# Kernel optimization log

Hardware: AMD Instinct MI355X
Metric: run time of the kernel (lower is better)

The kernel has to match this reference:

```python
import jax, jax.numpy as jnp
import numpy as np

B, C, H, W = 512, 512, 28, 28
HW = H * W


def setup_inputs() -> dict:
    key = jax.random.key(0)
    k1, k2, k3 = jax.random.split(key, 3)
    x = jax.random.normal(k1, (B, C, H, W), dtype=jnp.float32)
    # Per-channel Linear(HW -> 1): stacked weights (C, HW), biases (C,)
    bound = 1.0 / np.sqrt(HW)
    weight = jax.random.uniform(k2, (C, HW), minval=-bound, maxval=bound, dtype=jnp.float32)
    bias = jax.random.uniform(k3, (C,), minval=-bound, maxval=bound, dtype=jnp.float32)
    return {"x": x, "weight": weight, "bias": bias}


def reference(x, weight, bias):
    # x: (B, C, H, W) -> (B, C, HW); each channel c gets its own Linear(HW->1)
    xf = x.reshape(x.shape[0], C, HW)
    out = jnp.einsum('bcd,cd->bc', xf, weight) + bias  # (B, C)
    return out[:, :, None]  # (B, C, 1), matching torch.cat over channel dim
```

## Files before the change

kernel.cpp:

```cpp
#include <hip/hip_runtime.h>


#define NB 512
#define NC 512
#define NHW 784
#define NF4 196

__global__ __launch_bounds__(256) void rowdot_kernel(
    const float* __restrict__ x,
    const float* __restrict__ w,
    const float* __restrict__ bias,
    float* __restrict__ out)
{
    const int wave = threadIdx.x >> 6;
    const int lane = threadIdx.x & 63;
    const long long row = ((long long)blockIdx.x << 2) + wave;
    const int c = (int)(row & (NC - 1));

    const float4* __restrict__ xr = (const float4*)(x + row * (long long)NHW);
    const float4* __restrict__ wr = (const float4*)(w + (long long)c * NHW);

    float acc = 0.0f;
    #pragma unroll
    for (int k = 0; k < 3; ++k) {
        float4 a  = xr[lane + k * 64];
        float4 b4 = wr[lane + k * 64];
        acc += a.x * b4.x + a.y * b4.y + a.z * b4.z + a.w * b4.w;
    }
    if (lane < 4) {
        float4 a  = xr[192 + lane];
        float4 b4 = wr[192 + lane];
        acc += a.x * b4.x + a.y * b4.y + a.z * b4.z + a.w * b4.w;
    }

    #pragma unroll
    for (int off = 32; off > 0; off >>= 1)
        acc += __shfl_down(acc, off, 64);

    if (lane == 0)
        out[row] = acc + bias[c];
}

extern "C" void kernel_launch(void* const* d_in, const int* in_sizes, int n_in,
                              void* d_out, int out_size, void* d_ws, size_t ws_size,
                              hipStream_t stream) {
    const float* x    = (const float*)d_in[0];
    const float* w    = (const float*)d_in[1];
    const float* bias = (const float*)d_in[2];
    float* out        = (float*)d_out;

    const int rows = NB * NC;
    const int blocks = rows / 4;
    rowdot_kernel<<<blocks, 256, 0, stream>>>(x, w, bias, out);
}
```

Before: 1.006 ms.

## Make row-dot kernel persistent with register-resident weights and prefetched next row

Launches a fixed grid of 2048 blocks in which each wave handles 32 rows strided by 8192. Because that stride is a multiple of the channel count, every row a wave visits shares the same channel, so the channel's weights and bias are loaded into registers once. The next row's x is software-prefetched while the current dot product is reduced, and x is read with nontemporal loads. This is meant to cut redundant weight traffic and hide load latency, at the cost of fewer waves to cover latency and more register pressure.

```diff
diff --git a/kernel.cpp b/kernel.cpp
--- a/kernel.cpp
+++ b/kernel.cpp
@@ -1,10 +1,18 @@
 #include <hip/hip_runtime.h>
 
 
-#define NB 512
-#define NC 512
+typedef float v4 __attribute__((ext_vector_type(4)));
+
 #define NHW 784
-#define NF4 196
+#define NC  512
+#define ROWS (512 * 512)
+#define NBLK 2048
+#define WSTRIDE 8192
+#define ITERS 32
+
+__device__ __forceinline__ float dot4(v4 a, v4 b) {
+    return a.x * b.x + a.y * b.y + a.z * b.z + a.w * b.w;
+}
 
 __global__ __launch_bounds__(256) void rowdot_kernel(
     const float* __restrict__ x,
@@ -12,33 +20,46 @@
     const float* __restrict__ bias,
     float* __restrict__ out)
 {
-    const int wave = threadIdx.x >> 6;
     const int lane = threadIdx.x & 63;
-    const long long row = ((long long)blockIdx.x << 2) + wave;
-    const int c = (int)(row & (NC - 1));
+    const int wid  = (blockIdx.x << 2) + (threadIdx.x >> 6);
+    const int c    = wid & (NC - 1);
+    const int tidx = 192 + (lane & 3);
 
-    const float4* __restrict__ xr = (const float4*)(x + row * (long long)NHW);
-    const float4* __restrict__ wr = (const float4*)(w + (long long)c * NHW);
+    const v4* __restrict__ wr = (const v4*)(w + (long long)c * NHW);
+    v4 w0 = wr[lane];
+    v4 w1 = wr[lane + 64];
+    v4 w2 = wr[lane + 128];
+    v4 w3 = wr[tidx];
+    if (lane >= 4) { w3.x = 0.f; w3.y = 0.f; w3.z = 0.f; w3.w = 0.f; }
+    const float bc = bias[c];
 
-    float acc = 0.0f;
-    #pragma unroll
-    for (int k = 0; k < 3; ++k) {
-        float4 a  = xr[lane + k * 64];
-        float4 b4 = wr[lane + k * 64];
-        acc += a.x * b4.x + a.y * b4.y + a.z * b4.z + a.w * b4.w;
+    long long r = wid;
+    const v4* xr = (const v4*)(x + r * (long long)NHW);
+    v4 a0 = __builtin_nontemporal_load(xr + lane);
+    v4 a1 = __builtin_nontemporal_load(xr + lane + 64);
+    v4 a2 = __builtin_nontemporal_load(xr + lane + 128);
+    v4 a3 = __builtin_nontemporal_load(xr + tidx);
+
+    #pragma unroll 2
+    for (int i = 0; i < ITERS; ++i) {
+        const long long rn = (i + 1 < ITERS) ? r + WSTRIDE : r;
+        const v4* xn = (const v4*)(x + rn * (long long)NHW);
+        v4 b0 = __builtin_nontemporal_load(xn + lane);
+        v4 b1 = __builtin_nontemporal_load(xn + lane + 64);
+        v4 b2 = __builtin_nontemporal_load(xn + lane + 128);
+        v4 b3 = __builtin_nontemporal_load(xn + tidx);
+
+        float acc = dot4(a0, w0) + dot4(a1, w1) + dot4(a2, w2) + dot4(a3, w3);
+
+        #pragma unroll
+        for (int off = 32; off > 0; off >>= 1)
+            acc += __shfl_down(acc, off, 64);
+
+        if (lane == 0) out[r] = acc + bc;
+
+        a0 = b0; a1 = b1; a2 = b2; a3 = b3;
+        r = rn;
     }
-    if (lane < 4) {
-        float4 a  = xr[192 + lane];
-        float4 b4 = wr[192 + lane];
-        acc += a.x * b4.x + a.y * b4.y + a.z * b4.z + a.w * b4.w;
-    }
-
-    #pragma unroll
-    for (int off = 32; off > 0; off >>= 1)
-        acc += __shfl_down(acc, off, 64);
-
-    if (lane == 0)
-        out[row] = acc + bias[c];
 }
 
 extern "C" void kernel_launch(void* const* d_in, const int* in_sizes, int n_in,
@@ -49,7 +70,5 @@
     const float* bias = (const float*)d_in[2];
     float* out        = (float*)d_out;
 
-    const int rows = NB * NC;
-    const int blocks = rows / 4;
-    rowdot_kernel<<<blocks, 256, 0, stream>>>(x, w, bias, out);
+    rowdot_kernel<<<NBLK, 256, 0, stream>>>(x, w, bias, out);
 }
```

New measurement: 971.9 us. 3.4% less time.
